# Performance work log

Hardware: AMD Instinct MI355X
Metric: run time of the kernel (lower is better)

## Reference

```python
import jax, jax.numpy as jnp
import numpy as np

N, CIN, DIM, H, W = 16, 256, 32, 128, 128
NUMANGLE, NUMRHO = 192, 192
BN_EPS = 1e-5


def _conv(x, w, b, pad):
    y = jax.lax.conv_general_dilated(
        x, w, window_strides=(1, 1), padding=[(pad, pad), (pad, pad)],
        dimension_numbers=("NCHW", "OIHW", "NCHW"))
    return y + b[None, :, None, None]


def _bn_relu(x, gamma, beta):
    # training-mode batchnorm (batch statistics), as nn.BatchNorm2d in train()
    m = jnp.mean(x, axis=(0, 2, 3), keepdims=True)
    v = jnp.var(x, axis=(0, 2, 3), keepdims=True)
    y = (x - m) * jax.lax.rsqrt(v + BN_EPS)
    return jax.nn.relu(y * gamma[None, :, None, None] + beta[None, :, None, None])


def _rho_index():
    # LUT exactly as in the deep-hough-transform CUDA kernel
    irho = float(int(np.sqrt(H * H + W * W) + 1)) / (NUMRHO - 1)
    theta = np.arange(NUMANGLE) * (np.pi / NUMANGLE)
    tab_sin = np.sin(theta) / irho
    tab_cos = np.cos(theta) / irho
    xx = np.arange(W) - W // 2          # center-relative integer coords
    yy = np.arange(H) - H // 2
    # r[a, y, x] = round(x'*cos/irho + y'*sin/irho) + numrho/2
    r = np.round(xx[None, None, :] * tab_cos[:, None, None]
                 + yy[None, :, None] * tab_sin[:, None, None]).astype(np.int32)
    r = np.clip(r + NUMRHO // 2, 0, NUMRHO - 1)
    return jnp.asarray(r.reshape(NUMANGLE, H * W))  # [A, P]


_RHO_IDX = _rho_index()


def _dht(feat):
    # feat: [N, C, H, W] -> accumulator [N, C, numangle, numrho]
    n, c = feat.shape[0], feat.shape[1]
    feat_f = feat.reshape(n * c, H * W).T  # [P, N*C]

    def per_angle(idx):  # idx: [P] -> [numrho, N*C]
        return jax.ops.segment_sum(feat_f, idx, num_segments=NUMRHO)

    acc = jax.vmap(per_angle)(_RHO_IDX)  # [A, R, N*C]
    return acc.transpose(2, 0, 1).reshape(n, c, NUMANGLE, NUMRHO)


def setup_inputs() -> dict:
    key = jax.random.key(0)
    ks = jax.random.split(key, 8)
    s1 = 1.0 / np.sqrt(CIN)
    s3 = 1.0 / np.sqrt(DIM * 9)
    return {
        "x": jax.random.normal(ks[0], (N, CIN, H, W), jnp.float32),
        "w1": jax.random.normal(ks[1], (DIM, CIN, 1, 1), jnp.float32) * s1,
        "b1": jnp.zeros((DIM,), jnp.float32),
        "g1": jnp.ones((DIM,), jnp.float32),
        "be1": jnp.zeros((DIM,), jnp.float32),
        "w2": jax.random.normal(ks[2], (DIM, DIM, 3, 3), jnp.float32) * s3,
        "b2": jnp.zeros((DIM,), jnp.float32),
        "g2": jnp.ones((DIM,), jnp.float32),
        "be2": jnp.zeros((DIM,), jnp.float32),
        "w3": jax.random.normal(ks[3], (DIM, DIM, 3, 3), jnp.float32) * s3,
        "b3": jnp.zeros((DIM,), jnp.float32),
        "g3": jnp.ones((DIM,), jnp.float32),
        "be3": jnp.zeros((DIM,), jnp.float32),
    }


def reference(x, w1, b1, g1, be1, w2, b2, g2, be2, w3, b3, g3, be3):
    h = _bn_relu(_conv(x, w1, b1, 0), g1, be1)      # 1x1 conv + BN + ReLU
    a = _dht(h)                                      # deep Hough transform
    h = _bn_relu(_conv(a, w2, b2, 1), g2, be2)      # 3x3 conv + BN + ReLU
    h = _bn_relu(_conv(h, w3, b3, 1), g3, be3)      # 3x3 conv + BN + ReLU
    return h
```

## Files before the change

### kernel.cpp

```cpp
#include <hip/hip_runtime.h>
#include <hip/hip_fp16.h>
#include <math.h>

#define N_    16
#define CIN_  256
#define DIM_  32
#define H_    128
#define W_    128
#define P_    (H_*W_)
#define A_    192
#define R_    192
#define AR_   (A_*R_)
#define CSR_CAP 18432
#define NWORD 16520
#define SENT  16512

struct alignas(8) h4 { __half2 a, b; };

__device__ __forceinline__ int swz(int p) {
    int y = p >> 7, x = p & 127;
    return y * 129 + (x ^ ((y & 7) << 2));
}

__global__ __launch_bounds__(256) void csr_build(
        unsigned short* __restrict__ pix, int* __restrict__ offg) {
    int a = blockIdx.x;
    __shared__ int cnt[192];
    __shared__ int off[193];
    __shared__ unsigned char rho_s[P_];
    double theta = (double)a * (M_PI / 192.0);
    double irho  = 182.0 / 191.0;
    double ts = sin(theta) / irho;
    double tc = cos(theta) / irho;
    for (int i = threadIdx.x; i < 192; i += 256) cnt[i] = 0;
    __syncthreads();
    for (int p = threadIdx.x; p < P_; p += 256) {
        int y = p >> 7, x = p & 127;
        double v = __dadd_rn(__dmul_rn((double)(x - 64), tc),
                             __dmul_rn((double)(y - 64), ts));
        int r = (int)rint(v) + 96;
        r = r < 0 ? 0 : (r > 191 ? 191 : r);
        rho_s[p] = (unsigned char)r;
        atomicAdd(&cnt[r], 1);
    }
    __syncthreads();
    if (threadIdx.x == 0) {
        int run = 0;
        for (int r = 0; r < 192; ++r) { off[r] = run; run += (cnt[r] + 3) & ~3; }
        off[192] = run;
    }
    __syncthreads();
    if (threadIdx.x < 193) offg[a * 193 + threadIdx.x] = off[threadIdx.x];
    for (int i = threadIdx.x; i < 192; i += 256) cnt[i] = off[i];
    __syncthreads();
    unsigned short* pa = pix + (size_t)a * CSR_CAP;
    for (int p = threadIdx.x; p < P_; p += 256) {
        int idx = atomicAdd(&cnt[rho_s[p]], 1);
        pa[idx] = (unsigned short)swz(p);
    }
    __syncthreads();
    for (int r = threadIdx.x; r < 192; r += 256)
        for (int j = cnt[r]; j < off[r + 1]; ++j) pa[j] = SENT;
}

__global__ __launch_bounds__(256) void conv1x1_kernel(
        const float* __restrict__ x, const float* __restrict__ w,
        const float* __restrict__ b, float* __restrict__ out) {
    int g = blockIdx.x * 256 + threadIdx.x;
    int n = g >> 14, p = g & (P_ - 1);
    const float* xp = x + (size_t)n * CIN_ * P_ + p;
    float acc[DIM_];
    #pragma unroll
    for (int co = 0; co < DIM_; ++co) acc[co] = b[co];
    for (int ci = 0; ci < CIN_; ++ci) {
        float v = xp[(size_t)ci * P_];
        #pragma unroll
        for (int co = 0; co < DIM_; ++co)
            acc[co] += v * w[co * CIN_ + ci];
    }
    float* op = out + (size_t)n * DIM_ * P_ + p;
    #pragma unroll
    for (int co = 0; co < DIM_; ++co) op[(size_t)co * P_] = acc[co];
}

__global__ __launch_bounds__(256) void stats_kernel(
        const float* __restrict__ in, int S,
        double* __restrict__ dsum, double* __restrict__ dsq) {
    int c = blockIdx.x & 31;
    const float* p = in + (size_t)blockIdx.x * S;
    double s = 0.0, q = 0.0;
    for (int i = threadIdx.x; i < S; i += 256) {
        double v = (double)p[i];
        s += v; q += v * v;
    }
    #pragma unroll
    for (int off = 32; off > 0; off >>= 1) {
        s += __shfl_down(s, off, 64);
        q += __shfl_down(q, off, 64);
    }
    __shared__ double ls[4], lq[4];
    int wv = threadIdx.x >> 6;
    if ((threadIdx.x & 63) == 0) { ls[wv] = s; lq[wv] = q; }
    __syncthreads();
    if (threadIdx.x == 0) {
        s = ls[0] + ls[1] + ls[2] + ls[3];
        q = lq[0] + lq[1] + lq[2] + lq[3];
        atomicAdd(&dsum[c], s);
        atomicAdd(&dsq[c], q);
    }
}

__global__ void fin_kernel(const double* __restrict__ dsum, const double* __restrict__ dsq,
                           const float* __restrict__ g, const float* __restrict__ be,
                           double cnt, float* __restrict__ scsh) {
    int c = threadIdx.x;
    if (c < 32) {
        double m = dsum[c] / cnt;
        double v = dsq[c] / cnt - m * m;
        double rstd = 1.0 / sqrt(v + 1e-5);
        double sc = (double)g[c] * rstd;
        scsh[c]      = (float)sc;
        scsh[32 + c] = (float)((double)be[c] - m * sc);
    }
}

__global__ __launch_bounds__(1024) void dht_gather(
        const float* __restrict__ feat, const unsigned short* __restrict__ pix,
        const int* __restrict__ offg, const float* __restrict__ scsh,
        float one, float* __restrict__ acc) {
    extern __shared__ h4 d[];
    int quad = blockIdx.x >> 1, ah = blockIdx.x & 1;
    int nc0 = quad * 4;
    {
        int cb = nc0 & 31;
        float s0 = scsh[cb],     h0 = scsh[32 + cb];
        float s1 = scsh[cb + 1], h1 = scsh[33 + cb];
        float s2 = scsh[cb + 2], h2 = scsh[34 + cb];
        float s3 = scsh[cb + 3], h3 = scsh[35 + cb];
        const float4* f0p = (const float4*)(feat + (size_t)(nc0 + 0) * P_);
        const float4* f1p = (const float4*)(feat + (size_t)(nc0 + 1) * P_);
        const float4* f2p = (const float4*)(feat + (size_t)(nc0 + 2) * P_);
        const float4* f3p = (const float4*)(feat + (size_t)(nc0 + 3) * P_);
        for (int q = threadIdx.x; q < P_ / 4; q += 1024) {
            float4 a0 = f0p[q], a1 = f1p[q], a2 = f2p[q], a3 = f3p[q];
            int p = q * 4;
            int base = swz(p);
            h4 w;
            w.a = __halves2half2(__float2half(fmaxf(a0.x * s0 + h0, 0.f)),
                                 __float2half(fmaxf(a1.x * s1 + h1, 0.f)));
            w.b = __halves2half2(__float2half(fmaxf(a2.x * s2 + h2, 0.f)),
                                 __float2half(fmaxf(a3.x * s3 + h3, 0.f)));
            d[base + 0] = w;
            w.a = __halves2half2(__float2half(fmaxf(a0.y * s0 + h0, 0.f)),
                                 __float2half(fmaxf(a1.y * s1 + h1, 0.f)));
            w.b = __halves2half2(__float2half(fmaxf(a2.y * s2 + h2, 0.f)),
                                 __float2half(fmaxf(a3.y * s3 + h3, 0.f)));
            d[base + 1] = w;
            w.a = __halves2half2(__float2half(fmaxf(a0.z * s0 + h0, 0.f)),
                                 __float2half(fmaxf(a1.z * s1 + h1, 0.f)));
            w.b = __halves2half2(__float2half(fmaxf(a2.z * s2 + h2, 0.f)),
                                 __float2half(fmaxf(a3.z * s3 + h3, 0.f)));
            d[base + 2] = w;
            w.a = __halves2half2(__float2half(fmaxf(a0.w * s0 + h0, 0.f)),
                                 __float2half(fmaxf(a1.w * s1 + h1, 0.f)));
            w.b = __halves2half2(__float2half(fmaxf(a2.w * s2 + h2, 0.f)),
                                 __float2half(fmaxf(a3.w * s3 + h3, 0.f)));
            d[base + 3] = w;
        }
        if (threadIdx.x < 8) {
            *(uint2*)&d[SENT + threadIdx.x] = make_uint2(0u, 0u);
        }
    }
    __syncthreads();
    int abase = ah * 96;
    for (int it = 0; it < 18; ++it) {
        int seg = it * 1024 + threadIdx.x;
        int al = seg / 192, r = seg - al * 192;
        int a = abase + al;
        int o0 = offg[a * 193 + r];
        int o1 = offg[a * 193 + r + 1];
        const unsigned short* pl = pix + (size_t)a * CSR_CAP;
        float s0 = 0.f, s1 = 0.f, s2 = 0.f, s3 = 0.f;
        int j = o0;
        for (; j + 8 <= o1; j += 8) {
            ushort4 ua = *(const ushort4*)(pl + j);
            ushort4 ub = *(const ushort4*)(pl + j + 4);
            h4 v0 = d[ua.x];
            h4 v1 = d[ua.y];
            h4 v2 = d[ua.z];
            h4 v3 = d[ua.w];
            h4 v4 = d[ub.x];
            h4 v5 = d[ub.y];
            h4 v6 = d[ub.z];
            h4 v7 = d[ub.w];
            s0 += __low2float(v0.a) * one; s1 += __high2float(v0.a) * one;
            s2 += __low2float(v0.b) * one; s3 += __high2float(v0.b) * one;
            s0 += __low2float(v1.a) * one; s1 += __high2float(v1.a) * one;
            s2 += __low2float(v1.b) * one; s3 += __high2float(v1.b) * one;
            s0 += __low2float(v2.a) * one; s1 += __high2float(v2.a) * one;
            s2 += __low2float(v2.b) * one; s3 += __high2float(v2.b) * one;
            s0 += __low2float(v3.a) * one; s1 += __high2float(v3.a) * one;
            s2 += __low2float(v3.b) * one; s3 += __high2float(v3.b) * one;
            s0 += __low2float(v4.a) * one; s1 += __high2float(v4.a) * one;
            s2 += __low2float(v4.b) * one; s3 += __high2float(v4.b) * one;
            s0 += __low2float(v5.a) * one; s1 += __high2float(v5.a) * one;
            s2 += __low2float(v5.b) * one; s3 += __high2float(v5.b) * one;
            s0 += __low2float(v6.a) * one; s1 += __high2float(v6.a) * one;
            s2 += __low2float(v6.b) * one; s3 += __high2float(v6.b) * one;
            s0 += __low2float(v7.a) * one; s1 += __high2float(v7.a) * one;
            s2 += __low2float(v7.b) * one; s3 += __high2float(v7.b) * one;
        }
        if (j < o1) {
            ushort4 ua = *(const ushort4*)(pl + j);
            h4 v0 = d[ua.x];
            h4 v1 = d[ua.y];
            h4 v2 = d[ua.z];
            h4 v3 = d[ua.w];
            s0 += __low2float(v0.a) * one; s1 += __high2float(v0.a) * one;
            s2 += __low2float(v0.b) * one; s3 += __high2float(v0.b) * one;
            s0 += __low2float(v1.a) * one; s1 += __high2float(v1.a) * one;
            s2 += __low2float(v1.b) * one; s3 += __high2float(v1.b) * one;
            s0 += __low2float(v2.a) * one; s1 += __high2float(v2.a) * one;
            s2 += __low2float(v2.b) * one; s3 += __high2float(v2.b) * one;
            s0 += __low2float(v3.a) * one; s1 += __high2float(v3.a) * one;
            s2 += __low2float(v3.b) * one; s3 += __high2float(v3.b) * one;
        }
        size_t ob = (size_t)nc0 * AR_ + (size_t)a * R_ + r;
        acc[ob]           = s0;
        acc[ob + AR_]     = s1;
        acc[ob + 2 * AR_] = s2;
        acc[ob + 3 * AR_] = s3;
    }
}

template <bool BN>
__global__ __launch_bounds__(256) void conv3x3_kernel(
        const float* __restrict__ in, const float* __restrict__ w,
        const float* __restrict__ b,
        const float* __restrict__ sc, const float* __restrict__ sh,
        float* __restrict__ out) {
    __shared__ float tile[18][20];
    int tx = threadIdx.x & 15, ty = threadIdx.x >> 4;
    int x0 = blockIdx.x * 16, y0 = blockIdx.y * 16, n = blockIdx.z;
    float acc[DIM_];
    #pragma unroll
    for (int co = 0; co < DIM_; ++co) acc[co] = b[co];

    for (int ci = 0; ci < DIM_; ++ci) {
        __syncthreads();
        const float* src = in + ((size_t)(n * DIM_ + ci)) * AR_;
        float csc = BN ? sc[ci] : 0.f, csh = BN ? sh[ci] : 0.f;
        for (int t = threadIdx.x; t < 18 * 18; t += 256) {
            int ly = t / 18, lx = t - ly * 18;
            int gy = y0 - 1 + ly, gx = x0 - 1 + lx;
            float v = 0.f;
            if (gy >= 0 && gy < 192 && gx >= 0 && gx < 192) {
                v = src[gy * 192 + gx];
                if (BN) v = fmaxf(v * csc + csh, 0.f);
            }
            tile[ly][lx] = v;
        }
        __syncthreads();
        float v[9];
        #pragma unroll
        for (int k = 0; k < 9; ++k) v[k] = tile[ty + k / 3][tx + k % 3];
        const float* wp = w + ci * 9;
        #pragma unroll
        for (int co = 0; co < DIM_; ++co) {
            #pragma unroll
            for (int k = 0; k < 9; ++k)
                acc[co] += v[k] * wp[co * 288 + k];
        }
    }
    size_t o = ((size_t)(n * DIM_) * 192 + (y0 + ty)) * 192 + x0 + tx;
    #pragma unroll
    for (int co = 0; co < DIM_; ++co) out[o + (size_t)co * AR_] = acc[co];
}

__global__ __launch_bounds__(256) void bnrelu_kernel(
        const float* __restrict__ in, const float* __restrict__ scsh,
        float* __restrict__ out) {
    int i = blockIdx.x * 256 + threadIdx.x;
    if (i >= 4718592) return;
    int c = (i / 9216) & 31;
    float sc = scsh[c], sh = scsh[32 + c];
    float4 v = ((const float4*)in)[i];
    v.x = fmaxf(v.x * sc + sh, 0.f);
    v.y = fmaxf(v.y * sc + sh, 0.f);
    v.z = fmaxf(v.z * sc + sh, 0.f);
    v.w = fmaxf(v.w * sc + sh, 0.f);
    ((float4*)out)[i] = v;
}

extern "C" void kernel_launch(void* const* d_in, const int* in_sizes, int n_in,
                              void* d_out, int out_size, void* d_ws, size_t ws_size,
                              hipStream_t stream) {
    const float* x   = (const float*)d_in[0];
    const float* w1  = (const float*)d_in[1];
    const float* b1  = (const float*)d_in[2];
    const float* g1  = (const float*)d_in[3];
    const float* be1 = (const float*)d_in[4];
    const float* w2  = (const float*)d_in[5];
    const float* b2  = (const float*)d_in[6];
    const float* g2  = (const float*)d_in[7];
    const float* be2 = (const float*)d_in[8];
    const float* w3  = (const float*)d_in[9];
    const float* b3  = (const float*)d_in[10];
    const float* g3  = (const float*)d_in[11];
    const float* be3 = (const float*)d_in[12];
    float* out = (float*)d_out;

    char* ws = (char*)d_ws;
    float* bufA = (float*)(ws);
    unsigned short* pix = (unsigned short*)(ws + 33554432);
    int*   offg  = (int*)(ws + 40632320);
    float* bufB  = (float*)(ws + 75497472);
    double* stats = (double*)(ws + 150994944);
    float*  scsh  = (float*)(ws + 150996480);

    hipMemsetAsync(stats, 0, 192 * sizeof(double), stream);
    csr_build<<<192, 256, 0, stream>>>(pix, offg);

    conv1x1_kernel<<<1024, 256, 0, stream>>>(x, w1, b1, bufA);
    stats_kernel<<<512, 256, 0, stream>>>(bufA, P_, stats + 0, stats + 32);
    fin_kernel<<<1, 64, 0, stream>>>(stats + 0, stats + 32, g1, be1,
                                     (double)(N_ * P_), scsh);

    hipFuncSetAttribute((const void*)dht_gather,
                        hipFuncAttributeMaxDynamicSharedMemorySize,
                        NWORD * sizeof(h4));
    dht_gather<<<256, 1024, NWORD * sizeof(h4), stream>>>(
        bufA, pix, offg, scsh, 1.0f, bufB);

    conv3x3_kernel<false><<<dim3(12, 12, 16), 256, 0, stream>>>(
        bufB, w2, b2, nullptr, nullptr, bufA);
    stats_kernel<<<512, 256, 0, stream>>>(bufA, AR_, stats + 64, stats + 96);
    fin_kernel<<<1, 64, 0, stream>>>(stats + 64, stats + 96, g2, be2,
                                     (double)(N_ * AR_), scsh + 64);

    conv3x3_kernel<true><<<dim3(12, 12, 16), 256, 0, stream>>>(
        bufA, w3, b3, scsh + 64, scsh + 96, bufB);
    stats_kernel<<<512, 256, 0, stream>>>(bufB, AR_, stats + 128, stats + 160);
    fin_kernel<<<1, 64, 0, stream>>>(stats + 128, stats + 160, g3, be3,
                                     (double)(N_ * AR_), scsh + 128);

    bnrelu_kernel<<<18432, 256, 0, stream>>>(bufB, scsh + 128, out);
}
```

Baseline: 1.351 ms.

## Vectorize 1x1 conv, pre-sum halves in DHT gather, register-block and double-buffer 3x3 conv

The 1x1 conv now has each thread compute four pixels via float4 loads and stores, so each weight load is reused four times and the grid shrinks fourfold. In the DHT gather, values are first summed in half2 (groups of four) before conversion to float, which cuts conversion and add instructions but loses some precision in fp16 partial sums. The 3x3 conv now computes two output rows per thread with a 34-row tile. The next channel's tile is prefetched into registers and written to a second shared buffer, which halves the block count and removes one barrier per channel at the cost of higher register pressure.

```diff
diff --git a/kernel.cpp b/kernel.cpp
--- a/kernel.cpp
+++ b/kernel.cpp
@@ -67,20 +67,29 @@
         const float* __restrict__ x, const float* __restrict__ w,
         const float* __restrict__ b, float* __restrict__ out) {
     int g = blockIdx.x * 256 + threadIdx.x;
-    int n = g >> 14, p = g & (P_ - 1);
-    const float* xp = x + (size_t)n * CIN_ * P_ + p;
-    float acc[DIM_];
-    #pragma unroll
-    for (int co = 0; co < DIM_; ++co) acc[co] = b[co];
+    int n = g >> 12;
+    int q = g & 4095;
+    const float4* xp = (const float4*)(x + (size_t)n * CIN_ * P_) + q;
+    float4 acc[DIM_];
+    #pragma unroll
+    for (int co = 0; co < DIM_; ++co) {
+        float bb = b[co];
+        acc[co] = make_float4(bb, bb, bb, bb);
+    }
     for (int ci = 0; ci < CIN_; ++ci) {
-        float v = xp[(size_t)ci * P_];
+        float4 v = xp[(size_t)ci * (P_ / 4)];
         #pragma unroll
-        for (int co = 0; co < DIM_; ++co)
-            acc[co] += v * w[co * CIN_ + ci];
-    }
-    float* op = out + (size_t)n * DIM_ * P_ + p;
-    #pragma unroll
-    for (int co = 0; co < DIM_; ++co) op[(size_t)co * P_] = acc[co];
+        for (int co = 0; co < DIM_; ++co) {
+            float ww = w[co * CIN_ + ci];
+            acc[co].x += v.x * ww;
+            acc[co].y += v.y * ww;
+            acc[co].z += v.z * ww;
+            acc[co].w += v.w * ww;
+        }
+    }
+    float4* op = (float4*)(out + (size_t)n * DIM_ * P_) + q;
+    #pragma unroll
+    for (int co = 0; co < DIM_; ++co) op[(size_t)co * (P_ / 4)] = acc[co];
 }
 
 __global__ __launch_bounds__(256) void stats_kernel(
@@ -193,22 +202,14 @@
             h4 v5 = d[ub.y];
             h4 v6 = d[ub.z];
             h4 v7 = d[ub.w];
-            s0 += __low2float(v0.a) * one; s1 += __high2float(v0.a) * one;
-            s2 += __low2float(v0.b) * one; s3 += __high2float(v0.b) * one;
-            s0 += __low2float(v1.a) * one; s1 += __high2float(v1.a) * one;
-            s2 += __low2float(v1.b) * one; s3 += __high2float(v1.b) * one;
-            s0 += __low2float(v2.a) * one; s1 += __high2float(v2.a) * one;
-            s2 += __low2float(v2.b) * one; s3 += __high2float(v2.b) * one;
-            s0 += __low2float(v3.a) * one; s1 += __high2float(v3.a) * one;
-            s2 += __low2float(v3.b) * one; s3 += __high2float(v3.b) * one;
-            s0 += __low2float(v4.a) * one; s1 += __high2float(v4.a) * one;
-            s2 += __low2float(v4.b) * one; s3 += __high2float(v4.b) * one;
-            s0 += __low2float(v5.a) * one; s1 += __high2float(v5.a) * one;
-            s2 += __low2float(v5.b) * one; s3 += __high2float(v5.b) * one;
-            s0 += __low2float(v6.a) * one; s1 += __high2float(v6.a) * one;
-            s2 += __low2float(v6.b) * one; s3 += __high2float(v6.b) * one;
-            s0 += __low2float(v7.a) * one; s1 += __high2float(v7.a) * one;
-            s2 += __low2float(v7.b) * one; s3 += __high2float(v7.b) * one;
+            __half2 ta = __hadd2(__hadd2(v0.a, v1.a), __hadd2(v2.a, v3.a));
+            __half2 tb = __hadd2(__hadd2(v0.b, v1.b), __hadd2(v2.b, v3.b));
+            s0 += __low2float(ta) * one; s1 += __high2float(ta) * one;
+            s2 += __low2float(tb) * one; s3 += __high2float(tb) * one;
+            ta = __hadd2(__hadd2(v4.a, v5.a), __hadd2(v6.a, v7.a));
+            tb = __hadd2(__hadd2(v4.b, v5.b), __hadd2(v6.b, v7.b));
+            s0 += __low2float(ta) * one; s1 += __high2float(ta) * one;
+            s2 += __low2float(tb) * one; s3 += __high2float(tb) * one;
         }
         if (j < o1) {
             ushort4 ua = *(const ushort4*)(pl + j);
@@ -216,14 +217,10 @@
             h4 v1 = d[ua.y];
             h4 v2 = d[ua.z];
             h4 v3 = d[ua.w];
-            s0 += __low2float(v0.a) * one; s1 += __high2float(v0.a) * one;
-            s2 += __low2float(v0.b) * one; s3 += __high2float(v0.b) * one;
-            s0 += __low2float(v1.a) * one; s1 += __high2float(v1.a) * one;
-            s2 += __low2float(v1.b) * one; s3 += __high2float(v1.b) * one;
-            s0 += __low2float(v2.a) * one; s1 += __high2float(v2.a) * one;
-            s2 += __low2float(v2.b) * one; s3 += __high2float(v2.b) * one;
-            s0 += __low2float(v3.a) * one; s1 += __high2float(v3.a) * one;
-            s2 += __low2float(v3.b) * one; s3 += __high2float(v3.b) * one;
+            __half2 ta = __hadd2(__hadd2(v0.a, v1.a), __hadd2(v2.a, v3.a));
+            __half2 tb = __hadd2(__hadd2(v0.b, v1.b), __hadd2(v2.b, v3.b));
+            s0 += __low2float(ta) * one; s1 += __high2float(ta) * one;
+            s2 += __low2float(tb) * one; s3 += __high2float(tb) * one;
         }
         size_t ob = (size_t)nc0 * AR_ + (size_t)a * R_ + r;
         acc[ob]           = s0;
@@ -239,42 +236,76 @@
         const float* __restrict__ b,
         const float* __restrict__ sc, const float* __restrict__ sh,
         float* __restrict__ out) {
-    __shared__ float tile[18][20];
+    __shared__ float tile[2][34][20];
     int tx = threadIdx.x & 15, ty = threadIdx.x >> 4;
-    int x0 = blockIdx.x * 16, y0 = blockIdx.y * 16, n = blockIdx.z;
-    float acc[DIM_];
-    #pragma unroll
-    for (int co = 0; co < DIM_; ++co) acc[co] = b[co];
+    int x0 = blockIdx.x * 16, y0 = blockIdx.y * 32, n = blockIdx.z;
+    int tid = threadIdx.x;
+
+    float acc0[DIM_], acc1[DIM_];
+    #pragma unroll
+    for (int co = 0; co < DIM_; ++co) { acc0[co] = b[co]; acc1[co] = b[co]; }
+
+    auto ld = [&](int ci, int t) -> float {
+        int ly = t / 18, lx = t - ly * 18;
+        int gy = y0 - 1 + ly, gx = x0 - 1 + lx;
+        float v = 0.f;
+        if (gy >= 0 && gy < 192 && gx >= 0 && gx < 192) {
+            v = in[((size_t)(n * DIM_ + ci)) * AR_ + gy * 192 + gx];
+            if (BN) v = fmaxf(v * sc[ci] + sh[ci], 0.f);
+        }
+        return v;
+    };
+    auto st = [&](int buf, int t, float v) {
+        int ly = t / 18, lx = t - ly * 18;
+        tile[buf][ly][lx] = v;
+    };
+
+    {
+        float r0 = ld(0, tid), r1 = ld(0, tid + 256);
+        float r2 = (tid < 100) ? ld(0, tid + 512) : 0.f;
+        st(0, tid, r0); st(0, tid + 256, r1);
+        if (tid < 100) st(0, tid + 512, r2);
+    }
+    __syncthreads();
 
     for (int ci = 0; ci < DIM_; ++ci) {
-        __syncthreads();
-        const float* src = in + ((size_t)(n * DIM_ + ci)) * AR_;
-        float csc = BN ? sc[ci] : 0.f, csh = BN ? sh[ci] : 0.f;
-        for (int t = threadIdx.x; t < 18 * 18; t += 256) {
-            int ly = t / 18, lx = t - ly * 18;
-            int gy = y0 - 1 + ly, gx = x0 - 1 + lx;
-            float v = 0.f;
-            if (gy >= 0 && gy < 192 && gx >= 0 && gx < 192) {
-                v = src[gy * 192 + gx];
-                if (BN) v = fmaxf(v * csc + csh, 0.f);
-            }
-            tile[ly][lx] = v;
-        }
-        __syncthreads();
-        float v[9];
+        int cur = ci & 1, nxt = cur ^ 1;
+        float p0 = 0.f, p1 = 0.f, p2 = 0.f;
+        if (ci + 1 < DIM_) {
+            p0 = ld(ci + 1, tid);
+            p1 = ld(ci + 1, tid + 256);
+            if (tid < 100) p2 = ld(ci + 1, tid + 512);
+        }
+        float v[4][3];
         #pragma unroll
-        for (int k = 0; k < 9; ++k) v[k] = tile[ty + k / 3][tx + k % 3];
+        for (int rr = 0; rr < 4; ++rr)
+            #pragma unroll
+            for (int cc = 0; cc < 3; ++cc)
+                v[rr][cc] = tile[cur][2 * ty + rr][tx + cc];
         const float* wp = w + ci * 9;
         #pragma unroll
         for (int co = 0; co < DIM_; ++co) {
             #pragma unroll
-            for (int k = 0; k < 9; ++k)
-                acc[co] += v[k] * wp[co * 288 + k];
-        }
-    }
-    size_t o = ((size_t)(n * DIM_) * 192 + (y0 + ty)) * 192 + x0 + tx;
-    #pragma unroll
-    for (int co = 0; co < DIM_; ++co) out[o + (size_t)co * AR_] = acc[co];
+            for (int k = 0; k < 9; ++k) {
+                float ww = wp[co * 288 + k];
+                acc0[co] += v[k / 3][k % 3] * ww;
+                acc1[co] += v[k / 3 + 1][k % 3] * ww;
+            }
+        }
+        if (ci + 1 < DIM_) {
+            st(nxt, tid, p0); st(nxt, tid + 256, p1);
+            if (tid < 100) st(nxt, tid + 512, p2);
+        }
+        __syncthreads();
+    }
+
+    int oy = y0 + 2 * ty;
+    size_t o = ((size_t)(n * DIM_) * 192 + oy) * 192 + x0 + tx;
+    #pragma unroll
+    for (int co = 0; co < DIM_; ++co) {
+        out[o + (size_t)co * AR_]       = acc0[co];
+        out[o + 192 + (size_t)co * AR_] = acc1[co];
+    }
 }
 
 __global__ __launch_bounds__(256) void bnrelu_kernel(
@@ -321,7 +352,7 @@
     hipMemsetAsync(stats, 0, 192 * sizeof(double), stream);
     csr_build<<<192, 256, 0, stream>>>(pix, offg);
 
-    conv1x1_kernel<<<1024, 256, 0, stream>>>(x, w1, b1, bufA);
+    conv1x1_kernel<<<256, 256, 0, stream>>>(x, w1, b1, bufA);
     stats_kernel<<<512, 256, 0, stream>>>(bufA, P_, stats + 0, stats + 32);
     fin_kernel<<<1, 64, 0, stream>>>(stats + 0, stats + 32, g1, be1,
                                      (double)(N_ * P_), scsh);
@@ -332,13 +363,13 @@
     dht_gather<<<256, 1024, NWORD * sizeof(h4), stream>>>(
         bufA, pix, offg, scsh, 1.0f, bufB);
 
-    conv3x3_kernel<false><<<dim3(12, 12, 16), 256, 0, stream>>>(
+    conv3x3_kernel<false><<<dim3(12, 6, 16), 256, 0, stream>>>(
         bufB, w2, b2, nullptr, nullptr, bufA);
     stats_kernel<<<512, 256, 0, stream>>>(bufA, AR_, stats + 64, stats + 96);
     fin_kernel<<<1, 64, 0, stream>>>(stats + 64, stats + 96, g2, be2,
                                      (double)(N_ * AR_), scsh + 64);
 
-    conv3x3_kernel<true><<<dim3(12, 12, 16), 256, 0, stream>>>(
+    conv3x3_kernel<true><<<dim3(12, 6, 16), 256, 0, stream>>>(
         bufA, w3, b3, scsh + 64, scsh + 96, bufB);
     stats_kernel<<<512, 256, 0, stream>>>(bufB, AR_, stats + 128, stats + 160);
     fin_kernel<<<1, 64, 0, stream>>>(stats + 128, stats + 160, g3, be3,
```

After: 1.637 ms. 1.21x slower.
